# Kernel tuning notes

Measured on AMD Instinct MI355X. Metric: run time of the kernel, lower is better.

Reference implementation:

```python
import jax, jax.numpy as jnp
import numpy as np
from jax import lax

EPS = 1e-6

def ln_cf(x, w, b):
    # channels_first LayerNorm over dim 1 (biased variance, like the torch code)
    u = x.mean(1, keepdims=True)
    s = ((x - u) ** 2).mean(1, keepdims=True)
    return (x - u) / jnp.sqrt(s + EPS) * w[None, :, None, None] + b[None, :, None, None]

def dw3(x, w, b):
    # depthwise 3x3, stride 1, SAME padding; w: [C,1,3,3]
    C = x.shape[1]
    y = lax.conv_general_dilated(x, w, (1, 1), 'SAME',
                                 dimension_numbers=('NCHW', 'OIHW', 'NCHW'),
                                 feature_group_count=C)
    return y + b[None, :, None, None]

def pw(x, w, b):
    # 1x1 conv; w: [C_out, C_in]
    return jnp.einsum('bchw,oc->bohw', x, w) + b[None, :, None, None]

def shift_branch(x, sh, dw_w, dw_b, pw_w, pw_b):
    # pad -> roll -> crop == zero-fill shift by sh (|sh|=1)
    B, C, H, W = x.shape
    xp = jnp.pad(x, ((0, 0), (0, 0), (1, 1), (1, 1)))
    xs = jnp.roll(xp, shift=sh, axis=(2, 3))[:, :, 1:H + 1, 1:W + 1]
    return pw(jax.nn.gelu(dw3(xs, dw_w, dw_b), approximate=False), pw_w, pw_b)


def setup_inputs() -> dict:
    key = jax.random.key(0)
    B, C, H, W = 8, 128, 224, 224
    c = C // 4
    ks = jax.random.split(key, 32)
    d = {
        'x': jax.random.normal(ks[0], (B, C, H, W), jnp.float32),
        'n1_w': jnp.ones((C,), jnp.float32),
        'n1_b': jnp.zeros((C,), jnp.float32),
        'n2_w': jnp.ones((C,), jnp.float32),
        'n2_b': jnp.zeros((C,), jnp.float32),
        'c5_w': jax.random.normal(ks[1], (C, 1, 3, 3), jnp.float32) * 0.1,
        'c5_b': jax.random.normal(ks[2], (C,), jnp.float32) * 0.02,
        'ldw_dw_w': jax.random.normal(ks[3], (C, 1, 3, 3), jnp.float32) * 0.1,
        'ldw_dw_b': jax.random.normal(ks[4], (C,), jnp.float32) * 0.02,
        'ldw_pw_w': jax.random.normal(ks[5], (C, C), jnp.float32) * (1.0 / np.sqrt(C)),
        'ldw_pw_b': jax.random.normal(ks[6], (C,), jnp.float32) * 0.02,
    }
    for i in range(4):
        d[f's{i+1}_dw_w'] = jax.random.normal(ks[7 + 4 * i], (c, 1, 3, 3), jnp.float32) * 0.1
        d[f's{i+1}_dw_b'] = jax.random.normal(ks[8 + 4 * i], (c,), jnp.float32) * 0.02
        d[f's{i+1}_pw_w'] = jax.random.normal(ks[9 + 4 * i], (c, c), jnp.float32) * (1.0 / np.sqrt(c))
        d[f's{i+1}_pw_b'] = jax.random.normal(ks[10 + 4 * i], (c,), jnp.float32) * 0.02
    return d


def reference(x, n1_w, n1_b,
              s1_dw_w, s1_dw_b, s1_pw_w, s1_pw_b,
              s2_dw_w, s2_dw_b, s2_pw_w, s2_pw_b,
              s3_dw_w, s3_dw_b, s3_pw_w, s3_pw_b,
              s4_dw_w, s4_dw_b, s4_pw_w, s4_pw_b,
              c5_w, c5_b, n2_w, n2_b,
              ldw_dw_w, ldw_dw_b, ldw_pw_w, ldw_pw_b):
    x = ln_cf(x, n1_w, n1_b)
    C = x.shape[1]
    c = C // 4
    x1, x2, x3, x4 = jnp.split(x, 4, axis=1)
    # forward concat order: shift2(x2), shift4(x4), shift1(x1), shift3(x3)
    xshift = jnp.concatenate([
        shift_branch(x2, (-1, 1), s2_dw_w, s2_dw_b, s2_pw_w, s2_pw_b),
        shift_branch(x4, (1, -1), s4_dw_w, s4_dw_b, s4_pw_w, s4_pw_b),
        shift_branch(x1, (1, 1), s1_dw_w, s1_dw_b, s1_pw_w, s1_pw_b),
        shift_branch(x3, (-1, -1), s3_dw_w, s3_dw_b, s3_pw_w, s3_pw_b),
    ], axis=1)
    x = xshift + dw3(x, c5_w, c5_b)  # xres == x (cat of chunks)
    # channel shuffle with 2 groups
    B, Ct, H, W = x.shape
    x = x.reshape(B, 2, Ct // 2, H, W).transpose(0, 2, 1, 3, 4).reshape(B, Ct, H, W)
    x = ln_cf(x, n2_w, n2_b)
    x = pw(jax.nn.gelu(dw3(x, ldw_dw_w, ldw_dw_b), approximate=False), ldw_pw_w, ldw_pw_b)
    return x
```

## Files before the change

kernel.cpp:

```cpp
#include <hip/hip_runtime.h>
#include <hip/hip_bf16.h>
#include <math.h>

#define H_   224
#define W_   224
#define HWsz 50176
#define Cch  128

#define TAH 8
#define TAW 8
#define HAH 12
#define HAW 12
#define NHALO_A (HAH*HAW)

#define PBH 8
#define PBW 16
#define HBH 10
#define HBW 18
#define NHALO_B (HBH*HBW)
#define GPITCH 136

#define TPX 64

typedef __bf16 bf16x8 __attribute__((ext_vector_type(8)));
typedef float  f32x4  __attribute__((ext_vector_type(4)));

__device__ __forceinline__ float bf2f(__hip_bfloat16 v) { return __bfloat162float(v); }
__device__ __forceinline__ __hip_bfloat16 f2bf(float v) { return __float2bfloat16(v); }
__device__ __forceinline__ float ubf2f(unsigned short u) {
    unsigned x = ((unsigned)u) << 16; return __int_as_float((int)x);
}
__device__ __forceinline__ unsigned short f2ubf(float f) {
    __hip_bfloat16 h = __float2bfloat16(f);
    return *reinterpret_cast<unsigned short*>(&h);
}
__device__ __forceinline__ float gelu_exact(float x) {
    return 0.5f * x * (1.0f + erff(x * 0.70710678118654752440f));
}
__device__ __forceinline__ const float* rflp(const float* p) {
    unsigned long long v = (unsigned long long)p;
    unsigned lo = __builtin_amdgcn_readfirstlane((unsigned)v);
    unsigned hi = __builtin_amdgcn_readfirstlane((unsigned)(v >> 32));
    return (const float*)(((unsigned long long)hi << 32) | lo);
}

__global__ __launch_bounds__(256)
void prep(const float* __restrict__ ldww, float* __restrict__ dwT)
{
    const int i = blockIdx.x * 256 + threadIdx.x;
    if (i < 9 * Cch) {
        const int t = i >> 7, c = i & 127;
        dwT[i] = ldww[c * 9 + t];
    }
}

__global__ __launch_bounds__(256, 4)
void lnT(const float* __restrict__ x,
         const float* __restrict__ n1w, const float* __restrict__ n1b,
         unsigned int* __restrict__ y)
{
    __shared__ float xs[TPX][Cch + 1];
    __shared__ float rs_[4][TPX], rss_[4][TPX];
    __shared__ float2 st_s[TPX];

    const int t   = threadIdx.x;
    const int b   = blockIdx.y;
    const int sp0 = blockIdx.x * TPX;

    {
        const int lane = t & 63, wv = t >> 6;
        const float* xb = x + (size_t)b * Cch * HWsz + sp0 + lane;
        #pragma unroll 8
        for (int k = 0; k < 32; ++k) {
            const int c = wv * 32 + k;
            xs[lane][c] = xb[(size_t)c * HWsz];
        }
    }
    __syncthreads();

    {
        const int p = t & 63, q = t >> 6;
        float s = 0.f, ss = 0.f;
        #pragma unroll
        for (int k = 0; k < 32; ++k) {
            const float v = xs[p][q * 32 + k];
            s += v; ss += v * v;
        }
        rs_[q][p] = s; rss_[q][p] = ss;
    }
    __syncthreads();
    if (t < TPX) {
        const float S  = rs_[0][t] + rs_[1][t] + rs_[2][t] + rs_[3][t];
        const float SS = rss_[0][t] + rss_[1][t] + rss_[2][t] + rss_[3][t];
        const float mu  = S * (1.0f / 128.0f);
        const float var = SS * (1.0f / 128.0f) - mu * mu;
        st_s[t] = make_float2(mu, rsqrtf(var + 1e-6f));
    }
    __syncthreads();

    {
        const int ch = t & 15;
        const int pb = t >> 4;
        float w8[8], b8[8];
        #pragma unroll
        for (int j = 0; j < 8; ++j) {
            w8[j] = n1w[ch * 8 + j];
            b8[j] = n1b[ch * 8 + j];
        }
        #pragma unroll
        for (int it = 0; it < 4; ++it) {
            const int p = it * 16 + pb;
            const float2 st = st_s[p];
            unsigned int pk[4];
            #pragma unroll
            for (int u = 0; u < 4; ++u) {
                const int c0 = ch * 8 + u * 2;
                const float v0 = (xs[p][c0]     - st.x) * st.y * w8[u*2]   + b8[u*2];
                const float v1 = (xs[p][c0 + 1] - st.x) * st.y * w8[u*2+1] + b8[u*2+1];
                pk[u] = (unsigned int)f2ubf(v0) | ((unsigned int)f2ubf(v1) << 16);
            }
            *reinterpret_cast<uint4*>(y + ((size_t)b * HWsz + sp0 + p) * 64 + ch * 4) =
                make_uint4(pk[0], pk[1], pk[2], pk[3]);
        }
    }
}

__device__ __forceinline__ void conv_taps(
    float* __restrict__ G, const uint4* __restrict__ ys4,
    const float* __restrict__ w9,
    int rb, int cb, int chunkBase,
    const bool* rowOK, const bool* colOK, bool useMask)
{
    #pragma unroll
    for (int t3 = 0; t3 < 3; ++t3)
        #pragma unroll
        for (int t4 = 0; t4 < 3; ++t4) {
            const int tap = t3 * 3 + t4;
            int q = (rb + t3) * HAW + (cb + t4);
            if (useMask && !(rowOK[t3] && colOK[t4])) q = NHALO_A;
            const char* base = reinterpret_cast<const char*>(ys4) + q * 256;
            const int sw = q & 15;
            #pragma unroll
            for (int u = 0; u < 4; ++u) {
                const uint4 t = *reinterpret_cast<const uint4*>(
                                    base + (((chunkBase + u) ^ sw) << 4));
                const int i0 = u * 8;
                G[i0+0] = fmaf(w9[(i0+0)*9+tap], ubf2f((unsigned short)(t.x & 0xffffu)), G[i0+0]);
                G[i0+1] = fmaf(w9[(i0+1)*9+tap], ubf2f((unsigned short)(t.x >> 16)),     G[i0+1]);
                G[i0+2] = fmaf(w9[(i0+2)*9+tap], ubf2f((unsigned short)(t.y & 0xffffu)), G[i0+2]);
                G[i0+3] = fmaf(w9[(i0+3)*9+tap], ubf2f((unsigned short)(t.y >> 16)),     G[i0+3]);
                G[i0+4] = fmaf(w9[(i0+4)*9+tap], ubf2f((unsigned short)(t.z & 0xffffu)), G[i0+4]);
                G[i0+5] = fmaf(w9[(i0+5)*9+tap], ubf2f((unsigned short)(t.z >> 16)),     G[i0+5]);
                G[i0+6] = fmaf(w9[(i0+6)*9+tap], ubf2f((unsigned short)(t.w & 0xffffu)), G[i0+6]);
                G[i0+7] = fmaf(w9[(i0+7)*9+tap], ubf2f((unsigned short)(t.w >> 16)),     G[i0+7]);
            }
        }
}

__global__ __launch_bounds__(256, 3)
void kernelA(const unsigned short* __restrict__ y,
             const float* __restrict__ c5w, const float* __restrict__ c5b,
             const float* __restrict__ s1dw, const float* __restrict__ s1db,
             const float* __restrict__ s1pw, const float* __restrict__ s1pb,
             const float* __restrict__ s2dw, const float* __restrict__ s2db,
             const float* __restrict__ s2pw, const float* __restrict__ s2pb,
             const float* __restrict__ s3dw, const float* __restrict__ s3db,
             const float* __restrict__ s3pw, const float* __restrict__ s3pb,
             const float* __restrict__ s4dw, const float* __restrict__ s4db,
             const float* __restrict__ s4pw, const float* __restrict__ s4pb,
             unsigned int* __restrict__ zout, float2* __restrict__ st2)
{
    __shared__ uint4 y_s4[(NHALO_A + 1) * 16];
    __shared__ uint4 zx4[TAH * TAW * 16];

    const int tid = threadIdx.x;
    const int b   = blockIdx.z;
    const int h0  = blockIdx.y * TAH;
    const int w0  = blockIdx.x * TAW;

    {
        const int ch = tid & 15;
        const int pb = tid >> 4;
        #pragma unroll
        for (int it = 0; it < 9; ++it) {
            const int p  = it * 16 + pb;
            const int ph = p / HAW, pw2 = p - ph * HAW;
            const int gy = h0 - 2 + ph, gx = w0 - 2 + pw2;
            uint4 v = make_uint4(0u, 0u, 0u, 0u);
            if ((unsigned)gy < (unsigned)H_ && (unsigned)gx < (unsigned)W_)
                v = *reinterpret_cast<const uint4*>(
                    y + ((size_t)b * HWsz + (size_t)gy * W_ + gx) * Cch + ch * 8);
            y_s4[p * 16 + (ch ^ pb)] = v;
        }
        if (tid < 16) y_s4[NHALO_A * 16 + tid] = make_uint4(0u, 0u, 0u, 0u);
    }
    __syncthreads();

    {
        const int px  = tid & 63;
        const int k   = tid >> 6;
        const int py  = px >> 3, pxx = px & 7;
        const int gh  = h0 + py, gw = w0 + pxx;

        bool rowOK[3], colOK[3];
        #pragma unroll
        for (int t = 0; t < 3; ++t) {
            rowOK[t] = (gh - 1 + t >= 0) && (gh - 1 + t < H_);
            colOK[t] = (gw - 1 + t >= 0) && (gw - 1 + t < W_);
        }

        const float* dwW = rflp(k == 0 ? s1dw : k == 1 ? s2dw : k == 2 ? s3dw : s4dw);
        const float* dwB = rflp(k == 0 ? s1db : k == 1 ? s2db : k == 2 ? s3db : s4db);
        const float* pwW = rflp(k == 0 ? s1pw : k == 1 ? s2pw : k == 2 ? s3pw : s4pw);
        const float* pwB = rflp(k == 0 ? s1pb : k == 1 ? s2pb : k == 2 ? s3pb : s4pb);
        const int shh = (k == 0 || k == 3) ? 1 : -1;
        const int shw = (k <= 1) ? 1 : -1;
        const int ob  = (k == 0) ? 64 : (k == 1) ? 0 : (k == 2) ? 96 : 32;
        const float* c5wk = rflp(c5w + ob * 9);
        const float* c5bk = rflp(c5b + ob);

        float G[32], OV[32];

        #pragma unroll
        for (int i = 0; i < 32; ++i) G[i] = dwB[i];
        conv_taps(G, y_s4, dwW, py + 1 - shh, pxx + 1 - shw, k * 4, rowOK, colOK, true);
        #pragma unroll
        for (int i = 0; i < 32; ++i) G[i] = gelu_exact(G[i]);

        #pragma unroll 4
        for (int j = 0; j < 32; ++j) {
            float a = pwB[j] + c5bk[j];
            #pragma unroll
            for (int i = 0; i < 32; ++i)
                a = fmaf(pwW[j * 32 + i], G[i], a);
            OV[j] = a;
        }

        conv_taps(OV, y_s4, c5wk, py + 1, pxx + 1, ob >> 3, rowOK, colOK, false);

        const int sw = px & 15;
        #pragma unroll
        for (int u = 0; u < 4; ++u) {
            uint4 o;
            o.x = (unsigned)f2ubf(OV[u*8+0]) | ((unsigned)f2ubf(OV[u*8+1]) << 16);
            o.y = (unsigned)f2ubf(OV[u*8+2]) | ((unsigned)f2ubf(OV[u*8+3]) << 16);
            o.z = (unsigned)f2ubf(OV[u*8+4]) | ((unsigned)f2ubf(OV[u*8+5]) << 16);
            o.w = (unsigned)f2ubf(OV[u*8+6]) | ((unsigned)f2ubf(OV[u*8+7]) << 16);
            zx4[px * 16 + ((k * 4 + u) ^ sw)] = o;
        }
    }
    __syncthreads();

    {
        const int ppx = tid >> 2;
        const int s   = tid & 3;
        const int klo = (s < 2) ? 1 : 3;
        const int khi = (s < 2) ? 0 : 2;
        const int cb  = (s & 1) * 2;
        const int sw  = ppx & 15;

        const uint4 lo0 = zx4[ppx * 16 + ((klo * 4 + cb)     ^ sw)];
        const uint4 lo1 = zx4[ppx * 16 + ((klo * 4 + cb + 1) ^ sw)];
        const uint4 hi0 = zx4[ppx * 16 + ((khi * 4 + cb)     ^ sw)];
        const uint4 hi1 = zx4[ppx * 16 + ((khi * 4 + cb + 1) ^ sw)];

        uint4 o0, o1, o2, o3;
        o0.x = (lo0.x & 0xffffu) | (hi0.x << 16);
        o0.y = (lo0.x >> 16)     | (hi0.x & 0xffff0000u);
        o0.z = (lo0.y & 0xffffu) | (hi0.y << 16);
        o0.w = (lo0.y >> 16)     | (hi0.y & 0xffff0000u);
        o1.x = (lo0.z & 0xffffu) | (hi0.z << 16);
        o1.y = (lo0.z >> 16)     | (hi0.z & 0xffff0000u);
        o1.z = (lo0.w & 0xffffu) | (hi0.w << 16);
        o1.w = (lo0.w >> 16)     | (hi0.w & 0xffff0000u);
        o2.x = (lo1.x & 0xffffu) | (hi1.x << 16);
        o2.y = (lo1.x >> 16)     | (hi1.x & 0xffff0000u);
        o2.z = (lo1.y & 0xffffu) | (hi1.y << 16);
        o2.w = (lo1.y >> 16)     | (hi1.y & 0xffff0000u);
        o3.x = (lo1.z & 0xffffu) | (hi1.z << 16);
        o3.y = (lo1.z >> 16)     | (hi1.z & 0xffff0000u);
        o3.z = (lo1.w & 0xffffu) | (hi1.w << 16);
        o3.w = (lo1.w >> 16)     | (hi1.w & 0xffff0000u);

        const int gh = h0 + (ppx >> 3), gw = w0 + (ppx & 7);
        unsigned int* zp = zout + ((size_t)b * HWsz + (size_t)gh * W_ + gw) * 64 + s * 16;
        *reinterpret_cast<uint4*>(zp + 0)  = o0;
        *reinterpret_cast<uint4*>(zp + 4)  = o1;
        *reinterpret_cast<uint4*>(zp + 8)  = o2;
        *reinterpret_cast<uint4*>(zp + 12) = o3;

        float s1 = 0.f, s2 = 0.f;
        #define ACC(wrd) { const float fl = ubf2f((unsigned short)((wrd) & 0xffffu)); \
                           const float fh = ubf2f((unsigned short)((wrd) >> 16));     \
                           s1 += fl + fh; s2 += fl * fl + fh * fh; }
        ACC(o0.x) ACC(o0.y) ACC(o0.z) ACC(o0.w)
        ACC(o1.x) ACC(o1.y) ACC(o1.z) ACC(o1.w)
        ACC(o2.x) ACC(o2.y) ACC(o2.z) ACC(o2.w)
        ACC(o3.x) ACC(o3.y) ACC(o3.z) ACC(o3.w)
        #undef ACC

        s1 += __shfl_xor(s1, 1); s1 += __shfl_xor(s1, 2);
        s2 += __shfl_xor(s2, 1); s2 += __shfl_xor(s2, 2);
        if (s == 0) {
            const float mu  = s1 * (1.0f / 128.0f);
            const float var = s2 * (1.0f / 128.0f) - mu * mu;
            st2[(size_t)b * HWsz + (size_t)gh * W_ + gw] = make_float2(mu, rsqrtf(var + 1e-6f));
        }
    }
}

__global__ __launch_bounds__(256, 2)
void kernelB(const unsigned short* __restrict__ z, const float2* __restrict__ st2,
             const float* __restrict__ n2w, const float* __restrict__ n2b,
             const float* __restrict__ dwT, const float* __restrict__ dwB,
             const float* __restrict__ pwW, const float* __restrict__ pwB,
             float* __restrict__ out)
{
    __shared__ uint4 w_s4[NHALO_B * 16];
    __shared__ unsigned short g_s[PBH * PBW * GPITCH];

    const int tid  = threadIdx.x;
    const int lane = tid & 63;
    const int wv   = tid >> 6;
    const int b    = blockIdx.z;
    const int h0   = blockIdx.y * PBH;
    const int w0   = blockIdx.x * PBW;

    {
        const int ch = tid & 15;
        const int pb = tid >> 4;
        float nw[8], nb[8];
        #pragma unroll
        for (int j = 0; j < 8; ++j) {
            nw[j] = n2w[ch * 8 + j];
            nb[j] = n2b[ch * 8 + j];
        }
        #pragma unroll
        for (int it = 0; it < 12; ++it) {
            const int p = it * 16 + pb;
            if (p < NHALO_B) {
                const int ph = p / HBW, pw2 = p - ph * HBW;
                const int gy = h0 - 1 + ph, gx = w0 - 1 + pw2;
                uint4 o = make_uint4(0u, 0u, 0u, 0u);
                if ((unsigned)gy < (unsigned)H_ && (unsigned)gx < (unsigned)W_) {
                    const size_t pp = (size_t)b * HWsz + (size_t)gy * W_ + gx;
                    const uint4 zv = *reinterpret_cast<const uint4*>(z + pp * Cch + ch * 8);
                    const float2 st = st2[pp];
                    const float f0 = (ubf2f((unsigned short)(zv.x & 0xffffu)) - st.x) * st.y * nw[0] + nb[0];
                    const float f1 = (ubf2f((unsigned short)(zv.x >> 16))     - st.x) * st.y * nw[1] + nb[1];
                    const float f2 = (ubf2f((unsigned short)(zv.y & 0xffffu)) - st.x) * st.y * nw[2] + nb[2];
                    const float f3 = (ubf2f((unsigned short)(zv.y >> 16))     - st.x) * st.y * nw[3] + nb[3];
                    const float f4 = (ubf2f((unsigned short)(zv.z & 0xffffu)) - st.x) * st.y * nw[4] + nb[4];
                    const float f5 = (ubf2f((unsigned short)(zv.z >> 16))     - st.x) * st.y * nw[5] + nb[5];
                    const float f6 = (ubf2f((unsigned short)(zv.w & 0xffffu)) - st.x) * st.y * nw[6] + nb[6];
                    const float f7 = (ubf2f((unsigned short)(zv.w >> 16))     - st.x) * st.y * nw[7] + nb[7];
                    o.x = (unsigned)f2ubf(f0) | ((unsigned)f2ubf(f1) << 16);
                    o.y = (unsigned)f2ubf(f2) | ((unsigned)f2ubf(f3) << 16);
                    o.z = (unsigned)f2ubf(f4) | ((unsigned)f2ubf(f5) << 16);
                    o.w = (unsigned)f2ubf(f6) | ((unsigned)f2ubf(f7) << 16);
                }
                w_s4[p * 16 + (ch ^ (p & 15))] = o;
            }
        }
    }
    __syncthreads();

    {
        const int cc = lane & 15;
        const int sl = lane >> 4;
        const int s  = wv * 4 + sl;
        const int cbase = cc * 8;

        float db[8];
        float wt[9][8];
        #pragma unroll
        for (int j = 0; j < 8; ++j) db[j] = dwB[cbase + j];
        #pragma unroll
        for (int t = 0; t < 9; ++t)
            #pragma unroll
            for (int j = 0; j < 8; ++j)
                wt[t][j] = dwT[t * Cch + cbase + j];

        for (int r = 0; r < PBH; ++r) {
            float a[8];
            #pragma unroll
            for (int j = 0; j < 8; ++j) a[j] = db[j];

            #pragma unroll
            for (int dy = 0; dy < 3; ++dy)
                #pragma unroll
                for (int dx = 0; dx < 3; ++dx) {
                    const int tap = dy * 3 + dx;
                    const int q = (r + dy) * HBW + (s + dx);
                    const uint4 t4 = w_s4[q * 16 + (cc ^ (q & 15))];
                    a[0] = fmaf(wt[tap][0], ubf2f((unsigned short)(t4.x & 0xffffu)), a[0]);
                    a[1] = fmaf(wt[tap][1], ubf2f((unsigned short)(t4.x >> 16)),     a[1]);
                    a[2] = fmaf(wt[tap][2], ubf2f((unsigned short)(t4.y & 0xffffu)), a[2]);
                    a[3] = fmaf(wt[tap][3], ubf2f((unsigned short)(t4.y >> 16)),     a[3]);
                    a[4] = fmaf(wt[tap][4], ubf2f((unsigned short)(t4.z & 0xffffu)), a[4]);
                    a[5] = fmaf(wt[tap][5], ubf2f((unsigned short)(t4.z >> 16)),     a[5]);
                    a[6] = fmaf(wt[tap][6], ubf2f((unsigned short)(t4.w & 0xffffu)), a[6]);
                    a[7] = fmaf(wt[tap][7], ubf2f((unsigned short)(t4.w >> 16)),     a[7]);
                }

            unsigned int pk[4];
            #pragma unroll
            for (int q = 0; q < 4; ++q) {
                const unsigned short lo = f2ubf(gelu_exact(a[2*q]));
                const unsigned short hi = f2ubf(gelu_exact(a[2*q+1]));
                pk[q] = (unsigned int)lo | ((unsigned int)hi << 16);
            }
            const int row = r * PBW + s;
            const int boff = row * (GPITCH * 2) + ((cbase * 2) ^ ((row & 3) << 4));
            *reinterpret_cast<uint4*>(reinterpret_cast<char*>(g_s) + boff) =
                make_uint4(pk[0], pk[1], pk[2], pk[3]);
        }
    }
    __syncthreads();

    {
        const int ll = lane & 15;
        const int lh = lane >> 4;

        bf16x8 bfr[2][4];
        float  pb[2];
        #pragma unroll
        for (int t2 = 0; t2 < 2; ++t2) {
            const int o = (wv * 2 + t2) * 16 + ll;
            pb[t2] = pwB[o];
            #pragma unroll
            for (int kt = 0; kt < 4; ++kt) {
                const float* wp = pwW + (size_t)o * Cch + kt * 32 + lh * 8;
                bf16x8 vv;
                #pragma unroll
                for (int j = 0; j < 8; ++j) vv[j] = (__bf16)wp[j];
                bfr[t2][kt] = vv;
            }
        }

        #pragma unroll
        for (int r = 0; r < PBH; ++r) {
            const int row = r * PBW + ll;
            bf16x8 af[4];
            #pragma unroll
            for (int kt = 0; kt < 4; ++kt) {
                const int boff = row * (GPITCH * 2) + ((kt * 64 + lh * 16) ^ ((row & 3) << 4));
                af[kt] = *reinterpret_cast<const bf16x8*>(
                            reinterpret_cast<const char*>(g_s) + boff);
            }
            #pragma unroll
            for (int t2 = 0; t2 < 2; ++t2) {
                f32x4 acc = {0.f, 0.f, 0.f, 0.f};
                #pragma unroll
                for (int kt = 0; kt < 4; ++kt)
                    acc = __builtin_amdgcn_mfma_f32_16x16x32_bf16(af[kt], bfr[t2][kt], acc, 0, 0, 0);
                const int o = (wv * 2 + t2) * 16 + ll;
                float4 res = make_float4(acc[0] + pb[t2], acc[1] + pb[t2],
                                         acc[2] + pb[t2], acc[3] + pb[t2]);
                *reinterpret_cast<float4*>(
                    out + ((size_t)b * Cch + o) * HWsz + (size_t)(h0 + r) * W_ + w0 + lh * 4) = res;
            }
        }
    }
}

extern "C" void kernel_launch(void* const* d_in, const int* in_sizes, int n_in,
                              void* d_out, int out_size, void* d_ws, size_t ws_size,
                              hipStream_t stream)
{
    const float* x    = (const float*)d_in[0];
    const float* n1w  = (const float*)d_in[1];
    const float* n1b  = (const float*)d_in[2];
    const float* n2w  = (const float*)d_in[3];
    const float* n2b  = (const float*)d_in[4];
    const float* c5w  = (const float*)d_in[5];
    const float* c5b  = (const float*)d_in[6];
    const float* ldww = (const float*)d_in[7];
    const float* ldwb = (const float*)d_in[8];
    const float* lpww = (const float*)d_in[9];
    const float* lpwb = (const float*)d_in[10];
    const float* s1dw = (const float*)d_in[11];
    const float* s1db = (const float*)d_in[12];
    const float* s1pw = (const float*)d_in[13];
    const float* s1pb = (const float*)d_in[14];
    const float* s2dw = (const float*)d_in[15];
    const float* s2db = (const float*)d_in[16];
    const float* s2pw = (const float*)d_in[17];
    const float* s2pb = (const float*)d_in[18];
    const float* s3dw = (const float*)d_in[19];
    const float* s3db = (const float*)d_in[20];
    const float* s3pw = (const float*)d_in[21];
    const float* s3pb = (const float*)d_in[22];
    const float* s4dw = (const float*)d_in[23];
    const float* s4db = (const float*)d_in[24];
    const float* s4pw = (const float*)d_in[25];
    const float* s4pb = (const float*)d_in[26];

    const size_t yBytes  = (size_t)8 * Cch * HWsz * sizeof(unsigned short);
    const size_t zBytes  = yBytes;
    const size_t stBytes = (size_t)8 * HWsz * sizeof(float2);
    unsigned int*   y_u32 = (unsigned int*)d_ws;
    unsigned short* y_u16 = (unsigned short*)d_ws;
    unsigned int*   z_u32 = (unsigned int*)((char*)d_ws + yBytes);
    unsigned short* z_u16 = (unsigned short*)((char*)d_ws + yBytes);
    float2* st2 = (float2*)((char*)d_ws + yBytes + zBytes);
    float*  dwT = (float*)((char*)d_ws + yBytes + zBytes + stBytes);

    prep<<<dim3(5), 256, 0, stream>>>(ldww, dwT);
    lnT<<<dim3(HWsz / TPX, 8), 256, 0, stream>>>(x, n1w, n1b, y_u32);

    kernelA<<<dim3(W_ / TAW, H_ / TAH, 8), 256, 0, stream>>>(
        y_u16, c5w, c5b,
        s1dw, s1db, s1pw, s1pb,
        s2dw, s2db, s2pw, s2pb,
        s3dw, s3db, s3pw, s3pb,
        s4dw, s4db, s4pw, s4pb, z_u32, st2);

    kernelB<<<dim3(W_ / PBW, H_ / PBH, 8), 256, 0, stream>>>(
        z_u16, st2, n2w, n2b, dwT, ldwb, lpww, lpwb, (float*)d_out);
}
```

Before: 474.7 us.

## Use MFMA for shift-branch pointwise conv and move c5 depthwise after shuffle

Each wave's per-branch 32x32 pointwise conv in kernelA, previously scalar FMAs over registers, now runs on bf16 MFMA 16x16x32 instructions with GELU activations staged through shared memory. The c5 depthwise conv moves into the shuffle/store phase, where each thread handles 16+16 channels of one pixel, and LN statistics are reduced through shared memory instead of shuffles. This cuts VALU work and register pressure. The cost is extra barriers and bf16 rounding of the intermediate activations and weights.

Result: faster. 445.5 us (-6.2%).

```diff
diff --git a/kernel.cpp b/kernel.cpp
--- a/kernel.cpp
+++ b/kernel.cpp
@@ -42,6 +42,12 @@
     unsigned lo = __builtin_amdgcn_readfirstlane((unsigned)v);
     unsigned hi = __builtin_amdgcn_readfirstlane((unsigned)(v >> 32));
     return (const float*)(((unsigned long long)hi << 32) | lo);
+}
+__device__ __forceinline__ void unpack8(float* F, uint4 v) {
+    F[0] = ubf2f((unsigned short)(v.x & 0xffffu)); F[1] = ubf2f((unsigned short)(v.x >> 16));
+    F[2] = ubf2f((unsigned short)(v.y & 0xffffu)); F[3] = ubf2f((unsigned short)(v.y >> 16));
+    F[4] = ubf2f((unsigned short)(v.z & 0xffffu)); F[5] = ubf2f((unsigned short)(v.z >> 16));
+    F[6] = ubf2f((unsigned short)(v.w & 0xffffu)); F[7] = ubf2f((unsigned short)(v.w >> 16));
 }
 
 __global__ __launch_bounds__(256)
@@ -157,6 +163,36 @@
         }
 }
 
+__device__ __forceinline__ void conv16(
+    float* __restrict__ F, const uint4* __restrict__ ys4,
+    const float* __restrict__ w9,
+    int rb, int cbq, int chunkBase)
+{
+    #pragma unroll
+    for (int t3 = 0; t3 < 3; ++t3)
+        #pragma unroll
+        for (int t4 = 0; t4 < 3; ++t4) {
+            const int tap = t3 * 3 + t4;
+            const int q = (rb + t3) * HAW + (cbq + t4);
+            const char* base = reinterpret_cast<const char*>(ys4) + q * 256;
+            const int sw = q & 15;
+            #pragma unroll
+            for (int u = 0; u < 2; ++u) {
+                const uint4 t = *reinterpret_cast<const uint4*>(
+                                    base + (((chunkBase + u) ^ sw) << 4));
+                const int i0 = u * 8;
+                F[i0+0] = fmaf(w9[(i0+0)*9+tap], ubf2f((unsigned short)(t.x & 0xffffu)), F[i0+0]);
+                F[i0+1] = fmaf(w9[(i0+1)*9+tap], ubf2f((unsigned short)(t.x >> 16)),     F[i0+1]);
+                F[i0+2] = fmaf(w9[(i0+2)*9+tap], ubf2f((unsigned short)(t.y & 0xffffu)), F[i0+2]);
+                F[i0+3] = fmaf(w9[(i0+3)*9+tap], ubf2f((unsigned short)(t.y >> 16)),     F[i0+3]);
+                F[i0+4] = fmaf(w9[(i0+4)*9+tap], ubf2f((unsigned short)(t.z & 0xffffu)), F[i0+4]);
+                F[i0+5] = fmaf(w9[(i0+5)*9+tap], ubf2f((unsigned short)(t.z >> 16)),     F[i0+5]);
+                F[i0+6] = fmaf(w9[(i0+6)*9+tap], ubf2f((unsigned short)(t.w & 0xffffu)), F[i0+6]);
+                F[i0+7] = fmaf(w9[(i0+7)*9+tap], ubf2f((unsigned short)(t.w >> 16)),     F[i0+7]);
+            }
+        }
+}
+
 __global__ __launch_bounds__(256, 3)
 void kernelA(const unsigned short* __restrict__ y,
              const float* __restrict__ c5w, const float* __restrict__ c5b,
@@ -215,96 +251,131 @@
         const float* pwB = rflp(k == 0 ? s1pb : k == 1 ? s2pb : k == 2 ? s3pb : s4pb);
         const int shh = (k == 0 || k == 3) ? 1 : -1;
         const int shw = (k <= 1) ? 1 : -1;
-        const int ob  = (k == 0) ? 64 : (k == 1) ? 0 : (k == 2) ? 96 : 32;
-        const float* c5wk = rflp(c5w + ob * 9);
-        const float* c5bk = rflp(c5b + ob);
-
-        float G[32], OV[32];
-
+
+        float G[32];
         #pragma unroll
         for (int i = 0; i < 32; ++i) G[i] = dwB[i];
         conv_taps(G, y_s4, dwW, py + 1 - shh, pxx + 1 - shw, k * 4, rowOK, colOK, true);
         #pragma unroll
         for (int i = 0; i < 32; ++i) G[i] = gelu_exact(G[i]);
 
-        #pragma unroll 4
-        for (int j = 0; j < 32; ++j) {
-            float a = pwB[j] + c5bk[j];
-            #pragma unroll
-            for (int i = 0; i < 32; ++i)
-                a = fmaf(pwW[j * 32 + i], G[i], a);
-            OV[j] = a;
-        }
-
-        conv_taps(OV, y_s4, c5wk, py + 1, pxx + 1, ob >> 3, rowOK, colOK, false);
-
-        const int sw = px & 15;
-        #pragma unroll
-        for (int u = 0; u < 4; ++u) {
+        uint4* Gk = zx4 + k * 256;
+        #pragma unroll
+        for (int c = 0; c < 4; ++c) {
             uint4 o;
-            o.x = (unsigned)f2ubf(OV[u*8+0]) | ((unsigned)f2ubf(OV[u*8+1]) << 16);
-            o.y = (unsigned)f2ubf(OV[u*8+2]) | ((unsigned)f2ubf(OV[u*8+3]) << 16);
-            o.z = (unsigned)f2ubf(OV[u*8+4]) | ((unsigned)f2ubf(OV[u*8+5]) << 16);
-            o.w = (unsigned)f2ubf(OV[u*8+6]) | ((unsigned)f2ubf(OV[u*8+7]) << 16);
-            zx4[px * 16 + ((k * 4 + u) ^ sw)] = o;
-        }
-    }
-    __syncthreads();
-
-    {
-        const int ppx = tid >> 2;
-        const int s   = tid & 3;
+            o.x = (unsigned)f2ubf(G[c*8+0]) | ((unsigned)f2ubf(G[c*8+1]) << 16);
+            o.y = (unsigned)f2ubf(G[c*8+2]) | ((unsigned)f2ubf(G[c*8+3]) << 16);
+            o.z = (unsigned)f2ubf(G[c*8+4]) | ((unsigned)f2ubf(G[c*8+5]) << 16);
+            o.w = (unsigned)f2ubf(G[c*8+6]) | ((unsigned)f2ubf(G[c*8+7]) << 16);
+            Gk[px * 4 + (c ^ (px & 3))] = o;
+        }
+        __builtin_amdgcn_sched_barrier(0);
+
+        bf16x8 afr[2];
+        f32x4  acc[2][4];
+        #pragma unroll
+        for (int at = 0; at < 2; ++at) {
+            const float* wp = pwW + (at * 16 + (px & 15)) * 32 + (px >> 4) * 8;
+            const float4 wa = *reinterpret_cast<const float4*>(wp);
+            const float4 wb = *reinterpret_cast<const float4*>(wp + 4);
+            bf16x8 v;
+            v[0] = (__bf16)wa.x; v[1] = (__bf16)wa.y; v[2] = (__bf16)wa.z; v[3] = (__bf16)wa.w;
+            v[4] = (__bf16)wb.x; v[5] = (__bf16)wb.y; v[6] = (__bf16)wb.z; v[7] = (__bf16)wb.w;
+            afr[at] = v;
+            const float4 bi = *reinterpret_cast<const float4*>(pwB + at * 16 + (px >> 4) * 4);
+            #pragma unroll
+            for (int bt = 0; bt < 4; ++bt) {
+                acc[at][bt][0] = bi.x; acc[at][bt][1] = bi.y;
+                acc[at][bt][2] = bi.z; acc[at][bt][3] = bi.w;
+            }
+        }
+        #pragma unroll
+        for (int bt = 0; bt < 4; ++bt) {
+            const int p2 = bt * 16 + (px & 15);
+            const bf16x8 bfg = *reinterpret_cast<const bf16x8*>(
+                &Gk[p2 * 4 + ((px >> 4) ^ (px & 3))]);
+            #pragma unroll
+            for (int at = 0; at < 2; ++at)
+                acc[at][bt] = __builtin_amdgcn_mfma_f32_16x16x32_bf16(
+                                  afr[at], bfg, acc[at][bt], 0, 0, 0);
+        }
+        __syncthreads();
+
+        #pragma unroll
+        for (int at = 0; at < 2; ++at)
+            #pragma unroll
+            for (int bt = 0; bt < 4; ++bt) {
+                const int p2  = bt * 16 + (px & 15);
+                const int jj  = at * 16 + ((px >> 4) << 2);
+                const int ck  = k * 4 + (jj >> 3);
+                const int sub = (jj >> 2) & 1;
+                uint2 o;
+                o.x = (unsigned)f2ubf(acc[at][bt][0]) | ((unsigned)f2ubf(acc[at][bt][1]) << 16);
+                o.y = (unsigned)f2ubf(acc[at][bt][2]) | ((unsigned)f2ubf(acc[at][bt][3]) << 16);
+                *reinterpret_cast<uint2*>(
+                    reinterpret_cast<char*>(zx4) + p2 * 256 +
+                    ((ck ^ (p2 & 15)) << 4) + sub * 8) = o;
+            }
+    }
+    __syncthreads();
+
+    {
+        const int s   = tid >> 6;
+        const int p3  = tid & 63;
+        const int py3 = p3 >> 3, px3 = p3 & 7;
+        const int gh3 = h0 + py3, gw3 = w0 + px3;
+        const int sw  = p3 & 15;
         const int klo = (s < 2) ? 1 : 3;
         const int khi = (s < 2) ? 0 : 2;
         const int cb  = (s & 1) * 2;
-        const int sw  = ppx & 15;
-
-        const uint4 lo0 = zx4[ppx * 16 + ((klo * 4 + cb)     ^ sw)];
-        const uint4 lo1 = zx4[ppx * 16 + ((klo * 4 + cb + 1) ^ sw)];
-        const uint4 hi0 = zx4[ppx * 16 + ((khi * 4 + cb)     ^ sw)];
-        const uint4 hi1 = zx4[ppx * 16 + ((khi * 4 + cb + 1) ^ sw)];
-
-        uint4 o0, o1, o2, o3;
-        o0.x = (lo0.x & 0xffffu) | (hi0.x << 16);
-        o0.y = (lo0.x >> 16)     | (hi0.x & 0xffff0000u);
-        o0.z = (lo0.y & 0xffffu) | (hi0.y << 16);
-        o0.w = (lo0.y >> 16)     | (hi0.y & 0xffff0000u);
-        o1.x = (lo0.z & 0xffffu) | (hi0.z << 16);
-        o1.y = (lo0.z >> 16)     | (hi0.z & 0xffff0000u);
-        o1.z = (lo0.w & 0xffffu) | (hi0.w << 16);
-        o1.w = (lo0.w >> 16)     | (hi0.w & 0xffff0000u);
-        o2.x = (lo1.x & 0xffffu) | (hi1.x << 16);
-        o2.y = (lo1.x >> 16)     | (hi1.x & 0xffff0000u);
-        o2.z = (lo1.y & 0xffffu) | (hi1.y << 16);
-        o2.w = (lo1.y >> 16)     | (hi1.y & 0xffff0000u);
-        o3.x = (lo1.z & 0xffffu) | (hi1.z << 16);
-        o3.y = (lo1.z >> 16)     | (hi1.z & 0xffff0000u);
-        o3.z = (lo1.w & 0xffffu) | (hi1.w << 16);
-        o3.w = (lo1.w >> 16)     | (hi1.w & 0xffff0000u);
-
-        const int gh = h0 + (ppx >> 3), gw = w0 + (ppx & 7);
-        unsigned int* zp = zout + ((size_t)b * HWsz + (size_t)gh * W_ + gw) * 64 + s * 16;
-        *reinterpret_cast<uint4*>(zp + 0)  = o0;
-        *reinterpret_cast<uint4*>(zp + 4)  = o1;
-        *reinterpret_cast<uint4*>(zp + 8)  = o2;
-        *reinterpret_cast<uint4*>(zp + 12) = o3;
+
+        const uint4 lo0 = zx4[p3 * 16 + ((klo * 4 + cb)     ^ sw)];
+        const uint4 lo1 = zx4[p3 * 16 + ((klo * 4 + cb + 1) ^ sw)];
+        const uint4 hi0 = zx4[p3 * 16 + ((khi * 4 + cb)     ^ sw)];
+        const uint4 hi1 = zx4[p3 * 16 + ((khi * 4 + cb + 1) ^ sw)];
+        __syncthreads();
+
+        float Flo[16], Fhi[16];
+        unpack8(Flo,     lo0); unpack8(Flo + 8, lo1);
+        unpack8(Fhi,     hi0); unpack8(Fhi + 8, hi1);
+
+        const int obLo = (s < 2) ? 0  : 32;
+        const int obHi = (s < 2) ? 64 : 96;
+        const float* c5wL = rflp(c5w + (obLo + cb * 8) * 9);
+        const float* c5bL = rflp(c5b +  obLo + cb * 8);
+        const float* c5wH = rflp(c5w + (obHi + cb * 8) * 9);
+        const float* c5bH = rflp(c5b +  obHi + cb * 8);
+        #pragma unroll
+        for (int i = 0; i < 16; ++i) { Flo[i] += c5bL[i]; Fhi[i] += c5bH[i]; }
+        conv16(Flo, y_s4, c5wL, py3 + 1, px3 + 1, (obLo >> 3) + cb);
+        conv16(Fhi, y_s4, c5wH, py3 + 1, px3 + 1, (obHi >> 3) + cb);
 
         float s1 = 0.f, s2 = 0.f;
-        #define ACC(wrd) { const float fl = ubf2f((unsigned short)((wrd) & 0xffffu)); \
-                           const float fh = ubf2f((unsigned short)((wrd) >> 16));     \
-                           s1 += fl + fh; s2 += fl * fl + fh * fh; }
-        ACC(o0.x) ACC(o0.y) ACC(o0.z) ACC(o0.w)
-        ACC(o1.x) ACC(o1.y) ACC(o1.z) ACC(o1.w)
-        ACC(o2.x) ACC(o2.y) ACC(o2.z) ACC(o2.w)
-        ACC(o3.x) ACC(o3.y) ACC(o3.z) ACC(o3.w)
-        #undef ACC
-
-        s1 += __shfl_xor(s1, 1); s1 += __shfl_xor(s1, 2);
-        s2 += __shfl_xor(s2, 1); s2 += __shfl_xor(s2, 2);
+        unsigned pk[16];
+        #pragma unroll
+        for (int i = 0; i < 16; ++i) {
+            const unsigned short lo = f2ubf(Flo[i]);
+            const unsigned short hi = f2ubf(Fhi[i]);
+            const float fl = ubf2f(lo), fh = ubf2f(hi);
+            s1 += fl + fh; s2 += fl * fl + fh * fh;
+            pk[i] = (unsigned)lo | ((unsigned)hi << 16);
+        }
+        unsigned int* zp = zout + ((size_t)b * HWsz + (size_t)gh3 * W_ + gw3) * 64 + s * 16;
+        *reinterpret_cast<uint4*>(zp + 0)  = make_uint4(pk[0],  pk[1],  pk[2],  pk[3]);
+        *reinterpret_cast<uint4*>(zp + 4)  = make_uint4(pk[4],  pk[5],  pk[6],  pk[7]);
+        *reinterpret_cast<uint4*>(zp + 8)  = make_uint4(pk[8],  pk[9],  pk[10], pk[11]);
+        *reinterpret_cast<uint4*>(zp + 12) = make_uint4(pk[12], pk[13], pk[14], pk[15]);
+
+        float* red = reinterpret_cast<float*>(zx4);
+        red[s * 64 + p3]       = s1;
+        red[256 + s * 64 + p3] = s2;
+        __syncthreads();
         if (s == 0) {
-            const float mu  = s1 * (1.0f / 128.0f);
-            const float var = s2 * (1.0f / 128.0f) - mu * mu;
-            st2[(size_t)b * HWsz + (size_t)gh * W_ + gw] = make_float2(mu, rsqrtf(var + 1e-6f));
+            const float S  = red[p3] + red[64 + p3] + red[128 + p3] + red[192 + p3];
+            const float SS = red[256 + p3] + red[320 + p3] + red[384 + p3] + red[448 + p3];
+            const float mu  = S * (1.0f / 128.0f);
+            const float var = SS * (1.0f / 128.0f) - mu * mu;
+            st2[(size_t)b * HWsz + (size_t)gh3 * W_ + gw3] = make_float2(mu, rsqrtf(var + 1e-6f));
         }
     }
 }
```
